# Performance work log

Hardware: AMD Instinct MI355X
Metric: run time of the kernel (lower is better)

Reference implementation:

```python
import jax, jax.numpy as jnp
import numpy as np

B, N, IN_FEAT, OUT_FEAT, FEAT_DIM, N_HEAD = 16, 1024, 64, 128, 64, 4
NEG_SLOPE = 0.2


def setup_inputs() -> dict:
    key = jax.random.key(0)
    k1, k2, k3, k4 = jax.random.split(key, 4)
    # xavier-uniform-ish init, gain folded into scale
    def xav(k, shape):
        fan_in, fan_out = shape[-2], shape[-1]
        lim = 1.414 * np.sqrt(6.0 / (fan_in + fan_out))
        return jax.random.uniform(k, shape, jnp.float32, -lim, lim)
    return {
        "h": jax.random.normal(k1, (B, N, IN_FEAT), jnp.float32),
        "mask": jnp.ones((B, 1, N, N), jnp.float32),
        "w": xav(k2, (N_HEAD, IN_FEAT, OUT_FEAT)),
        "a_src": xav(k3, (N_HEAD, OUT_FEAT, FEAT_DIM)),
        "a_dst": xav(k4, (N_HEAD, OUT_FEAT, FEAT_DIM)),
        "bias": jnp.zeros((OUT_FEAT,), jnp.float32),
    }


def reference(h, mask, w, a_src, a_dst, bias):
    # h: [B,N,F_in]; w: [H,F_in,F_out] -> h_prime: [B,H,N,F_out]
    h_prime = jnp.einsum('bnf,hfo->bhno', h, w)
    attn_src = jnp.einsum('bhno,hod->bhnd', h_prime, a_src)  # [B,H,N,D]
    attn_dst = jnp.einsum('bhno,hod->bhnd', h_prime, a_dst)  # [B,H,N,D]
    scores = jnp.einsum('bhnd,bhmd->bhnm', attn_src, attn_dst)  # [B,H,N,N]
    attn = jax.nn.softmax(jax.nn.leaky_relu(scores, NEG_SLOPE), axis=-1)
    # dropout is identity in eval mode (deterministic reference)
    attn = attn * mask  # mask broadcast over heads
    out = jnp.einsum('bhnm,bhmo->bno', attn, h_prime) + bias  # sum over heads
    out = out + h_prime.sum(axis=1)  # skip connection
    return out, attn
```

## Files before the change

kernel.cpp:

```cpp
#include <hip/hip_runtime.h>

#define BB 16
#define NN 1024
#define FIN 64
#define FOUT 128
#define DD 64
#define HH 4
#define NEG 0.2f

#define RT 32
#define RT2 16
#define CT 128

typedef __attribute__((ext_vector_type(8))) short short8;
typedef __attribute__((ext_vector_type(4))) float f32x4;

__device__ __forceinline__ unsigned short f2bf(float x) {
    union { float f; unsigned u; } v; v.f = x;
    unsigned r = v.u + 0x7fffu + ((v.u >> 16) & 1u);
    return (unsigned short)(r >> 16);
}
__device__ __forceinline__ float bf2f(unsigned short s) {
    union { float f; unsigned u; } v; v.u = ((unsigned)s) << 16;
    return v.f;
}

#define MFMA(a, b, c) __builtin_amdgcn_mfma_f32_16x16x32_bf16((a), (b), (c), 0, 0, 0)

__global__ __launch_bounds__(256) void gat_k1(
    const float* __restrict__ h,
    const float* __restrict__ w,
    const float* __restrict__ a_src,
    const float* __restrict__ a_dst,
    unsigned short* __restrict__ asHg,
    unsigned short* __restrict__ asLg,
    unsigned short* __restrict__ adHg,
    unsigned short* __restrict__ adLg,
    unsigned short* __restrict__ hpPg,
    float* __restrict__ hpsum)
{
    __shared__ float hL[RT][FIN + 1];
    __shared__ float wL[FIN][FOUT + 2];
    __shared__ float hpL[RT][FOUT + 2];

    const int t  = threadIdx.x;
    const int tx = t & 31;
    const int ty = t >> 5;
    const int blk = blockIdx.x;
    const int b   = blk / (NN / RT);
    const int n0  = (blk % (NN / RT)) * RT;

    for (int idx = t; idx < RT * FIN / 4; idx += 256) {
        int r = (idx * 4) / FIN;
        int f = (idx * 4) % FIN;
        float4 v = *reinterpret_cast<const float4*>(&h[((size_t)b * NN + n0 + r) * FIN + f]);
        hL[r][f + 0] = v.x; hL[r][f + 1] = v.y; hL[r][f + 2] = v.z; hL[r][f + 3] = v.w;
    }

    float sum_acc[4][4];
#pragma unroll
    for (int i = 0; i < 4; i++)
#pragma unroll
        for (int j = 0; j < 4; j++) sum_acc[i][j] = 0.f;

    for (int hh = 0; hh < HH; ++hh) {
        __syncthreads();
        for (int idx = t; idx < FIN * FOUT / 4; idx += 256) {
            int k = (idx * 4) / FOUT;
            int o = (idx * 4) % FOUT;
            float4 v = *reinterpret_cast<const float4*>(&w[((size_t)hh * FIN + k) * FOUT + o]);
            wL[k][o + 0] = v.x; wL[k][o + 1] = v.y; wL[k][o + 2] = v.z; wL[k][o + 3] = v.w;
        }
        __syncthreads();

        float acc[4][4];
#pragma unroll
        for (int i = 0; i < 4; i++)
#pragma unroll
            for (int j = 0; j < 4; j++) acc[i][j] = 0.f;

#pragma unroll 8
        for (int k = 0; k < FIN; k++) {
            float av0 = hL[ty][k], av1 = hL[ty + 8][k], av2 = hL[ty + 16][k], av3 = hL[ty + 24][k];
            float bv0 = wL[k][tx], bv1 = wL[k][tx + 32], bv2 = wL[k][tx + 64], bv3 = wL[k][tx + 96];
            acc[0][0] += av0 * bv0; acc[0][1] += av0 * bv1; acc[0][2] += av0 * bv2; acc[0][3] += av0 * bv3;
            acc[1][0] += av1 * bv0; acc[1][1] += av1 * bv1; acc[1][2] += av1 * bv2; acc[1][3] += av1 * bv3;
            acc[2][0] += av2 * bv0; acc[2][1] += av2 * bv1; acc[2][2] += av2 * bv2; acc[2][3] += av2 * bv3;
            acc[3][0] += av3 * bv0; acc[3][1] += av3 * bv1; acc[3][2] += av3 * bv2; acc[3][3] += av3 * bv3;
        }

        const size_t bh = (size_t)b * HH + hh;
#pragma unroll
        for (int i = 0; i < 4; i++) {
            int r = i * 8 + ty;
#pragma unroll
            for (int j = 0; j < 4; j++) {
                int o = j * 32 + tx;
                hpL[r][o] = acc[i][j];
                sum_acc[i][j] += acc[i][j];
            }
        }
        __syncthreads();

        float as0[4], as1[4], ad0[4], ad1[4];
#pragma unroll
        for (int i = 0; i < 4; i++) { as0[i] = 0.f; as1[i] = 0.f; ad0[i] = 0.f; ad1[i] = 0.f; }

#pragma unroll 4
        for (int o = 0; o < FOUT; o++) {
            size_t aoff = ((size_t)hh * FOUT + o) * DD;
            float sv0 = a_src[aoff + tx];
            float sv1 = a_src[aoff + tx + 32];
            float dv0 = a_dst[aoff + tx];
            float dv1 = a_dst[aoff + tx + 32];
#pragma unroll
            for (int i = 0; i < 4; i++) {
                float hv = hpL[i * 8 + ty][o];
                as0[i] += hv * sv0; as1[i] += hv * sv1;
                ad0[i] += hv * dv0; ad1[i] += hv * dv1;
            }
        }
#pragma unroll
        for (int i = 0; i < 4; i++) {
            int r = i * 8 + ty;
            size_t base = (bh * NN + n0 + r) * DD;
            unsigned short h0, h1;
            h0 = f2bf(as0[i]); asHg[base + tx]      = h0; asLg[base + tx]      = f2bf(as0[i] - bf2f(h0));
            h1 = f2bf(as1[i]); asHg[base + tx + 32] = h1; asLg[base + tx + 32] = f2bf(as1[i] - bf2f(h1));
            h0 = f2bf(ad0[i]); adHg[base + tx]      = h0; adLg[base + tx]      = f2bf(ad0[i] - bf2f(h0));
            h1 = f2bf(ad1[i]); adHg[base + tx + 32] = h1; adLg[base + tx + 32] = f2bf(ad1[i] - bf2f(h1));
        }

        {
            int o = t & 127, half = t >> 7;
            size_t dst = ((bh * (NN / 32) + (n0 >> 5)) * FOUT + o) * 32 + half * 16;
            short8 v0, v1;
#pragma unroll
            for (int k = 0; k < 8; k++) v0[k] = (short)f2bf(hpL[half * 16 + k][o]);
#pragma unroll
            for (int k = 0; k < 8; k++) v1[k] = (short)f2bf(hpL[half * 16 + 8 + k][o]);
            *reinterpret_cast<short8*>(&hpPg[dst])     = v0;
            *reinterpret_cast<short8*>(&hpPg[dst + 8]) = v1;
        }
    }

#pragma unroll
    for (int i = 0; i < 4; i++) {
        int r = i * 8 + ty;
        size_t rowoff = ((size_t)b * NN + n0 + r) * FOUT;
#pragma unroll
        for (int j = 0; j < 4; j++) {
            hpsum[rowoff + j * 32 + tx] = sum_acc[i][j];
        }
    }
}

__global__ __launch_bounds__(256) void gat_k2(
    const float* __restrict__ mask,
    const float* __restrict__ bias,
    const unsigned short* __restrict__ asHg,
    const unsigned short* __restrict__ asLg,
    const unsigned short* __restrict__ adHg,
    const unsigned short* __restrict__ adLg,
    const unsigned short* __restrict__ hpPg,
    const float* __restrict__ hpsum,
    float* __restrict__ out,
    float* __restrict__ attn)
{
    __shared__ __align__(16) unsigned char smem[8192 + 512];
    unsigned short* pBs0 = reinterpret_cast<unsigned short*>(smem);
    unsigned short* pBs1 = reinterpret_cast<unsigned short*>(smem + 4096);
    float*          redm = reinterpret_cast<float*>(smem + 8192);
    float*          redl = reinterpret_cast<float*>(smem + 8192 + 256);
    float*          outL = reinterpret_cast<float*>(smem);

    const int t  = threadIdx.x;
    const int l  = t & 63;
    const int w  = t >> 6;
    const int li = l & 15;
    const int g  = l >> 4;

    const int lb = (blockIdx.x & 7) * 128 + (blockIdx.x >> 3);
    const int b  = lb >> 6;
    const int n0 = (lb & 63) * RT2;

    f32x4 oacc[2];
    oacc[0] = f32x4{0.f, 0.f, 0.f, 0.f};
    oacc[1] = f32x4{0.f, 0.f, 0.f, 0.f};

    for (int hh = 0; hh < HH; hh++) {
        const size_t bh = (size_t)b * HH + hh;

        short8 aH[2], aL[2];
#pragma unroll
        for (int ks = 0; ks < 2; ks++) {
            size_t src = (bh * NN + n0 + li) * DD + ks * 32 + g * 8;
            aH[ks] = *reinterpret_cast<const short8*>(&asHg[src]);
            aL[ks] = *reinterpret_cast<const short8*>(&asLg[src]);
        }

        const unsigned short* adHb = adHg + bh * NN * DD;
        const unsigned short* adLb = adLg + bh * NN * DD;

        float sc[8][2][4];
#pragma unroll
        for (int ct = 0; ct < 8; ct++) {
#pragma unroll
            for (int cf = 0; cf < 2; cf++) {
                short8 bHr[2], bLr[2];
#pragma unroll
                for (int ks = 0; ks < 2; ks++) {
                    size_t off = (size_t)(ct * CT + w * 32 + cf * 16 + li) * DD + ks * 32 + g * 8;
                    bHr[ks] = *reinterpret_cast<const short8*>(&adHb[off]);
                    bLr[ks] = *reinterpret_cast<const short8*>(&adLb[off]);
                }
                f32x4 s = f32x4{0.f, 0.f, 0.f, 0.f};
                __builtin_amdgcn_s_setprio(1);
#pragma unroll
                for (int ks = 0; ks < 2; ks++) {
                    s = MFMA(aH[ks], bHr[ks], s);
                    s = MFMA(aH[ks], bLr[ks], s);
                    s = MFMA(aL[ks], bHr[ks], s);
                }
                __builtin_amdgcn_s_setprio(0);
#pragma unroll
                for (int q = 0; q < 4; q++) {
                    float v = s[q];
                    sc[ct][cf][q] = v > 0.f ? v : NEG * v;
                }
            }
        }

        float mreg[4];
#pragma unroll
        for (int q = 0; q < 4; q++) {
            float m = sc[0][0][q];
#pragma unroll
            for (int ct = 0; ct < 8; ct++)
                m = fmaxf(m, fmaxf(sc[ct][0][q], sc[ct][1][q]));
#pragma unroll
            for (int msk = 1; msk < 16; msk <<= 1)
                m = fmaxf(m, __shfl_xor(m, msk));
            mreg[q] = m;
        }
        __syncthreads();
        if (li == 0) {
#pragma unroll
            for (int q = 0; q < 4; q++) redm[w * 16 + g * 4 + q] = mreg[q];
        }
        __syncthreads();
        float mf[4];
#pragma unroll
        for (int q = 0; q < 4; q++) {
            int row = g * 4 + q;
            mf[q] = fmaxf(fmaxf(redm[row], redm[16 + row]),
                          fmaxf(redm[32 + row], redm[48 + row]));
        }
        float lreg[4] = {0.f, 0.f, 0.f, 0.f};
#pragma unroll
        for (int ct = 0; ct < 8; ct++)
#pragma unroll
            for (int cf = 0; cf < 2; cf++)
#pragma unroll
                for (int q = 0; q < 4; q++) {
                    float e = __expf(sc[ct][cf][q] - mf[q]);
                    sc[ct][cf][q] = e;
                    lreg[q] += e;
                }
#pragma unroll
        for (int q = 0; q < 4; q++) {
#pragma unroll
            for (int msk = 1; msk < 16; msk <<= 1)
                lreg[q] += __shfl_xor(lreg[q], msk);
        }
        if (li == 0) {
#pragma unroll
            for (int q = 0; q < 4; q++) redl[w * 16 + g * 4 + q] = lreg[q];
        }
        __syncthreads();
        float linv[4];
#pragma unroll
        for (int q = 0; q < 4; q++) {
            int row = g * 4 + q;
            linv[q] = 1.0f / (redl[row] + redl[16 + row] + redl[32 + row] + redl[48 + row]);
        }

        const unsigned short* hpbase = hpPg + bh * (size_t)(NN / 32) * FOUT * 32;
#pragma unroll
        for (int ct = 0; ct < 8; ct++) {
            float mvv[2][4];
#pragma unroll
            for (int cf = 0; cf < 2; cf++)
#pragma unroll
                for (int q = 0; q < 4; q++)
                    mvv[cf][q] = mask[((size_t)b * NN + n0 + g * 4 + q) * NN
                                      + ct * CT + w * 32 + cf * 16 + li];

            unsigned short* pB = (ct & 1) ? pBs1 : pBs0;
            float pm[2][4];
#pragma unroll
            for (int cf = 0; cf < 2; cf++)
#pragma unroll
                for (int q = 0; q < 4; q++) {
                    int row = g * 4 + q;
                    int cl  = w * 32 + cf * 16 + li;
                    float pmv = sc[ct][cf][q] * linv[q] * mvv[cf][q];
                    attn[(bh * NN + n0 + row) * NN + ct * CT + cl] = pmv;
                    pm[cf][q] = pmv;
                }
#pragma unroll
            for (int cf = 0; cf < 2; cf++)
#pragma unroll
                for (int q = 0; q < 4; q++) {
                    int row = g * 4 + q;
                    int cl  = w * 32 + cf * 16 + li;
                    pB[row * 128 + (cl ^ (row * 8))] = f2bf(pm[cf][q]);
                }

            const unsigned short* hpb = hpbase + (size_t)ct * 4 * FOUT * 32;
            short8 hbv[4][2];
#pragma unroll
            for (int kc = 0; kc < 4; kc++) {
                hbv[kc][0] = *reinterpret_cast<const short8*>(
                    &hpb[((size_t)kc * FOUT + w * 32 + li) * 32 + g * 8]);
                hbv[kc][1] = *reinterpret_cast<const short8*>(
                    &hpb[((size_t)kc * FOUT + w * 32 + 16 + li) * 32 + g * 8]);
            }
            asm volatile("s_waitcnt lgkmcnt(0)\n\ts_barrier" ::: "memory");

#pragma unroll
            for (int kc = 0; kc < 4; kc++) {
                int k = kc * 32 + g * 8;
                short8 pa = *reinterpret_cast<const short8*>(&pB[li * 128 + (k ^ (li * 8))]);
                __builtin_amdgcn_s_setprio(1);
                oacc[0] = MFMA(pa, hbv[kc][0], oacc[0]);
                oacc[1] = MFMA(pa, hbv[kc][1], oacc[1]);
                __builtin_amdgcn_s_setprio(0);
            }
        }
    }

    __syncthreads();
#pragma unroll
    for (int of = 0; of < 2; of++)
#pragma unroll
        for (int q = 0; q < 4; q++) {
            int row = g * 4 + q;
            int col = w * 32 + of * 16 + li;
            outL[row * 128 + col] = oacc[of][q];
        }
    __syncthreads();
    {
        int row = t >> 4, cb = (t & 15) * 8;
        size_t obase = ((size_t)b * NN + n0 + row) * FOUT + cb;
#pragma unroll
        for (int k4 = 0; k4 < 2; k4++) {
            float4 v  = *reinterpret_cast<float4*>(&outL[row * 128 + cb + k4 * 4]);
            float4 bs = *reinterpret_cast<const float4*>(&bias[cb + k4 * 4]);
            float4 hs = *reinterpret_cast<const float4*>(&hpsum[obase + k4 * 4]);
            v.x += bs.x + hs.x; v.y += bs.y + hs.y; v.z += bs.z + hs.z; v.w += bs.w + hs.w;
            *reinterpret_cast<float4*>(&out[obase + k4 * 4]) = v;
        }
    }
}

extern "C" void kernel_launch(void* const* d_in, const int* in_sizes, int n_in,
                              void* d_out, int out_size, void* d_ws, size_t ws_size,
                              hipStream_t stream) {
    const float* h      = (const float*)d_in[0];
    const float* mask   = (const float*)d_in[1];
    const float* w      = (const float*)d_in[2];
    const float* a_src  = (const float*)d_in[3];
    const float* a_dst  = (const float*)d_in[4];
    const float* bias   = (const float*)d_in[5];

    float* out  = (float*)d_out;
    float* attn = out + (size_t)BB * NN * FOUT;

    const size_t NASD = (size_t)BB * HH * NN * DD;
    unsigned short* asHg = (unsigned short*)d_ws;
    unsigned short* asLg = asHg + NASD;
    unsigned short* adHg = asLg + NASD;
    unsigned short* adLg = adHg + NASD;
    unsigned short* hpPg = adLg + NASD;
    float* hpsum = (float*)(hpPg + (size_t)BB * HH * FOUT * NN);

    dim3 block(256);
    gat_k1<<<dim3(BB * (NN / RT)),  block, 0, stream>>>(h, w, a_src, a_dst, asHg, asLg, adHg, adLg, hpPg, hpsum);
    gat_k2<<<dim3(BB * (NN / RT2)), block, 0, stream>>>(mask, bias, asHg, asLg, adHg, adLg, hpPg, hpsum, out, attn);
}
```

Measured before the change: 387.3 us.

## Use online softmax with bf16-packed exponentials and transposed score MFMA in attention kernel

Swaps the score MFMA operands so each lane owns one query row, which allows float4 mask loads and float4 attn stores. Replaces the two-pass max/sum reduction with an online per-tile max and rescaled sum, merged across lanes and waves as (max, sum) pairs in a single shared-memory round. Keeps the exponentials packed as bf16 to cut register use and adds a launch bound of 3 blocks per SM. It also splits the h' loads so half are issued inside the MFMA loop. The aim is higher occupancy, fewer barriers and wider global stores, at the cost of bf16 rounding of the exponentials before they are written to attn.

```diff
diff --git a/kernel.cpp b/kernel.cpp
--- a/kernel.cpp
+++ b/kernel.cpp
@@ -23,6 +23,9 @@
 __device__ __forceinline__ float bf2f(unsigned short s) {
     union { float f; unsigned u; } v; v.u = ((unsigned)s) << 16;
     return v.f;
+}
+__device__ __forceinline__ unsigned pack2bf(float lo, float hi) {
+    return (unsigned)f2bf(lo) | ((unsigned)f2bf(hi) << 16);
 }
 
 #define MFMA(a, b, c) __builtin_amdgcn_mfma_f32_16x16x32_bf16((a), (b), (c), 0, 0, 0)
@@ -155,7 +158,7 @@
     }
 }
 
-__global__ __launch_bounds__(256) void gat_k2(
+__global__ __launch_bounds__(256, 3) void gat_k2(
     const float* __restrict__ mask,
     const float* __restrict__ bias,
     const unsigned short* __restrict__ asHg,
@@ -170,8 +173,7 @@
     __shared__ __align__(16) unsigned char smem[8192 + 512];
     unsigned short* pBs0 = reinterpret_cast<unsigned short*>(smem);
     unsigned short* pBs1 = reinterpret_cast<unsigned short*>(smem + 4096);
-    float*          redm = reinterpret_cast<float*>(smem + 8192);
-    float*          redl = reinterpret_cast<float*>(smem + 8192 + 256);
+    float2*         red  = reinterpret_cast<float2*>(smem + 8192);
     float*          outL = reinterpret_cast<float*>(smem);
 
     const int t  = threadIdx.x;
@@ -179,6 +181,7 @@
     const int w  = t >> 6;
     const int li = l & 15;
     const int g  = l >> 4;
+    const int colb = w * 32;
 
     const int lb = (blockIdx.x & 7) * 128 + (blockIdx.x >> 3);
     const int b  = lb >> 6;
@@ -202,134 +205,114 @@
         const unsigned short* adHb = adHg + bh * NN * DD;
         const unsigned short* adLb = adLg + bh * NN * DD;
 
-        float sc[8][2][4];
+        float m = -3.0e38f, lsum = 0.f;
+        float mL[8];
+        unsigned pk[8][2][2];
 #pragma unroll
         for (int ct = 0; ct < 8; ct++) {
+            float sv[2][4];
 #pragma unroll
             for (int cf = 0; cf < 2; cf++) {
-                short8 bHr[2], bLr[2];
+                short8 xH[2], xL[2];
 #pragma unroll
                 for (int ks = 0; ks < 2; ks++) {
-                    size_t off = (size_t)(ct * CT + w * 32 + cf * 16 + li) * DD + ks * 32 + g * 8;
-                    bHr[ks] = *reinterpret_cast<const short8*>(&adHb[off]);
-                    bLr[ks] = *reinterpret_cast<const short8*>(&adLb[off]);
+                    size_t off = (size_t)(ct * CT + colb + cf * 16 + li) * DD + ks * 32 + g * 8;
+                    xH[ks] = *reinterpret_cast<const short8*>(&adHb[off]);
+                    xL[ks] = *reinterpret_cast<const short8*>(&adLb[off]);
                 }
                 f32x4 s = f32x4{0.f, 0.f, 0.f, 0.f};
                 __builtin_amdgcn_s_setprio(1);
 #pragma unroll
                 for (int ks = 0; ks < 2; ks++) {
-                    s = MFMA(aH[ks], bHr[ks], s);
-                    s = MFMA(aH[ks], bLr[ks], s);
-                    s = MFMA(aL[ks], bHr[ks], s);
+                    s = MFMA(xH[ks], aH[ks], s);
+                    s = MFMA(xH[ks], aL[ks], s);
+                    s = MFMA(xL[ks], aH[ks], s);
                 }
                 __builtin_amdgcn_s_setprio(0);
 #pragma unroll
                 for (int q = 0; q < 4; q++) {
                     float v = s[q];
-                    sc[ct][cf][q] = v > 0.f ? v : NEG * v;
+                    sv[cf][q] = v > 0.f ? v : NEG * v;
                 }
             }
-        }
-
-        float mreg[4];
-#pragma unroll
-        for (int q = 0; q < 4; q++) {
-            float m = sc[0][0][q];
-#pragma unroll
-            for (int ct = 0; ct < 8; ct++)
-                m = fmaxf(m, fmaxf(sc[ct][0][q], sc[ct][1][q]));
-#pragma unroll
-            for (int msk = 1; msk < 16; msk <<= 1)
-                m = fmaxf(m, __shfl_xor(m, msk));
-            mreg[q] = m;
-        }
-        __syncthreads();
-        if (li == 0) {
-#pragma unroll
-            for (int q = 0; q < 4; q++) redm[w * 16 + g * 4 + q] = mreg[q];
-        }
-        __syncthreads();
-        float mf[4];
-#pragma unroll
-        for (int q = 0; q < 4; q++) {
-            int row = g * 4 + q;
-            mf[q] = fmaxf(fmaxf(redm[row], redm[16 + row]),
-                          fmaxf(redm[32 + row], redm[48 + row]));
-        }
-        float lreg[4] = {0.f, 0.f, 0.f, 0.f};
-#pragma unroll
-        for (int ct = 0; ct < 8; ct++)
+            float tm = sv[0][0];
 #pragma unroll
             for (int cf = 0; cf < 2; cf++)
 #pragma unroll
-                for (int q = 0; q < 4; q++) {
-                    float e = __expf(sc[ct][cf][q] - mf[q]);
-                    sc[ct][cf][q] = e;
-                    lreg[q] += e;
-                }
-#pragma unroll
-        for (int q = 0; q < 4; q++) {
-#pragma unroll
-            for (int msk = 1; msk < 16; msk <<= 1)
-                lreg[q] += __shfl_xor(lreg[q], msk);
-        }
-        if (li == 0) {
-#pragma unroll
-            for (int q = 0; q < 4; q++) redl[w * 16 + g * 4 + q] = lreg[q];
-        }
-        __syncthreads();
-        float linv[4];
-#pragma unroll
-        for (int q = 0; q < 4; q++) {
-            int row = g * 4 + q;
-            linv[q] = 1.0f / (redl[row] + redl[16 + row] + redl[32 + row] + redl[48 + row]);
+                for (int q = 0; q < 4; q++) tm = fmaxf(tm, sv[cf][q]);
+            float nm = fmaxf(m, tm);
+            lsum *= __expf(m - nm);
+            m = nm;
+            mL[ct] = nm;
+#pragma unroll
+            for (int cf = 0; cf < 2; cf++) {
+                float e0 = __expf(sv[cf][0] - nm);
+                float e1 = __expf(sv[cf][1] - nm);
+                float e2 = __expf(sv[cf][2] - nm);
+                float e3 = __expf(sv[cf][3] - nm);
+                lsum += (e0 + e1) + (e2 + e3);
+                pk[ct][cf][0] = pack2bf(e0, e1);
+                pk[ct][cf][1] = pack2bf(e2, e3);
+            }
+        }
+
+#pragma unroll
+        for (int msk = 16; msk <= 32; msk <<= 1) {
+            float om = __shfl_xor(m, msk);
+            float ol = __shfl_xor(lsum, msk);
+            float nm = fmaxf(m, om);
+            lsum = lsum * __expf(m - nm) + ol * __expf(om - nm);
+            m = nm;
+        }
+        __syncthreads();
+        if (g == 0) red[w * 16 + li] = make_float2(m, lsum);
+        __syncthreads();
+        float mf, linv;
+        {
+            float2 r0 = red[li], r1 = red[16 + li], r2 = red[32 + li], r3 = red[48 + li];
+            mf = fmaxf(fmaxf(r0.x, r1.x), fmaxf(r2.x, r3.x));
+            float ls = r0.y * __expf(r0.x - mf) + r1.y * __expf(r1.x - mf)
+                     + r2.y * __expf(r2.x - mf) + r3.y * __expf(r3.x - mf);
+            linv = 1.0f / ls;
         }
 
         const unsigned short* hpbase = hpPg + bh * (size_t)(NN / 32) * FOUT * 32;
 #pragma unroll
         for (int ct = 0; ct < 8; ct++) {
-            float mvv[2][4];
-#pragma unroll
-            for (int cf = 0; cf < 2; cf++)
-#pragma unroll
-                for (int q = 0; q < 4; q++)
-                    mvv[cf][q] = mask[((size_t)b * NN + n0 + g * 4 + q) * NN
-                                      + ct * CT + w * 32 + cf * 16 + li];
-
+            const float corr = __expf(mL[ct] - mf) * linv;
             unsigned short* pB = (ct & 1) ? pBs1 : pBs0;
-            float pm[2][4];
-#pragma unroll
-            for (int cf = 0; cf < 2; cf++)
-#pragma unroll
-                for (int q = 0; q < 4; q++) {
-                    int row = g * 4 + q;
-                    int cl  = w * 32 + cf * 16 + li;
-                    float pmv = sc[ct][cf][q] * linv[q] * mvv[cf][q];
-                    attn[(bh * NN + n0 + row) * NN + ct * CT + cl] = pmv;
-                    pm[cf][q] = pmv;
-                }
-#pragma unroll
-            for (int cf = 0; cf < 2; cf++)
-#pragma unroll
-                for (int q = 0; q < 4; q++) {
-                    int row = g * 4 + q;
-                    int cl  = w * 32 + cf * 16 + li;
-                    pB[row * 128 + (cl ^ (row * 8))] = f2bf(pm[cf][q]);
-                }
+#pragma unroll
+            for (int cf = 0; cf < 2; cf++) {
+                int c = ct * CT + colb + cf * 16 + g * 4;
+                float4 mv = *reinterpret_cast<const float4*>(
+                    &mask[((size_t)b * NN + n0 + li) * NN + c]);
+                float p0 = bf2f((unsigned short)(pk[ct][cf][0] & 0xffff)) * corr * mv.x;
+                float p1 = bf2f((unsigned short)(pk[ct][cf][0] >> 16))    * corr * mv.y;
+                float p2 = bf2f((unsigned short)(pk[ct][cf][1] & 0xffff)) * corr * mv.z;
+                float p3 = bf2f((unsigned short)(pk[ct][cf][1] >> 16))    * corr * mv.w;
+                float4 av; av.x = p0; av.y = p1; av.z = p2; av.w = p3;
+                *reinterpret_cast<float4*>(
+                    &attn[(bh * NN + n0 + li) * NN + c]) = av;
+                int c0 = colb + cf * 16 + g * 4;
+                uint2 pw;
+                pw.x = pack2bf(p0, p1);
+                pw.y = pack2bf(p2, p3);
+                *reinterpret_cast<uint2*>(&pB[li * 128 + (c0 ^ (li * 8))]) = pw;
+            }
 
             const unsigned short* hpb = hpbase + (size_t)ct * 4 * FOUT * 32;
-            short8 hbv[4][2];
-#pragma unroll
-            for (int kc = 0; kc < 4; kc++) {
+            short8 hbv[2][2];
+#pragma unroll
+            for (int kc = 0; kc < 2; kc++) {
                 hbv[kc][0] = *reinterpret_cast<const short8*>(
-                    &hpb[((size_t)kc * FOUT + w * 32 + li) * 32 + g * 8]);
+                    &hpb[((size_t)kc * FOUT + colb + li) * 32 + g * 8]);
                 hbv[kc][1] = *reinterpret_cast<const short8*>(
-                    &hpb[((size_t)kc * FOUT + w * 32 + 16 + li) * 32 + g * 8]);
+                    &hpb[((size_t)kc * FOUT + colb + 16 + li) * 32 + g * 8]);
             }
             asm volatile("s_waitcnt lgkmcnt(0)\n\ts_barrier" ::: "memory");
 
 #pragma unroll
-            for (int kc = 0; kc < 4; kc++) {
+            for (int kc = 0; kc < 2; kc++) {
                 int k = kc * 32 + g * 8;
                 short8 pa = *reinterpret_cast<const short8*>(&pB[li * 128 + (k ^ (li * 8))]);
                 __builtin_amdgcn_s_setprio(1);
@@ -337,6 +320,19 @@
                 oacc[1] = MFMA(pa, hbv[kc][1], oacc[1]);
                 __builtin_amdgcn_s_setprio(0);
             }
+#pragma unroll
+            for (int kc = 2; kc < 4; kc++) {
+                int k = kc * 32 + g * 8;
+                short8 pa = *reinterpret_cast<const short8*>(&pB[li * 128 + (k ^ (li * 8))]);
+                short8 h0 = *reinterpret_cast<const short8*>(
+                    &hpb[((size_t)kc * FOUT + colb + li) * 32 + g * 8]);
+                short8 h1 = *reinterpret_cast<const short8*>(
+                    &hpb[((size_t)kc * FOUT + colb + 16 + li) * 32 + g * 8]);
+                __builtin_amdgcn_s_setprio(1);
+                oacc[0] = MFMA(pa, h0, oacc[0]);
+                oacc[1] = MFMA(pa, h1, oacc[1]);
+                __builtin_amdgcn_s_setprio(0);
+            }
         }
     }
 
@@ -346,7 +342,7 @@
 #pragma unroll
         for (int q = 0; q < 4; q++) {
             int row = g * 4 + q;
-            int col = w * 32 + of * 16 + li;
+            int col = colb + of * 16 + li;
             outL[row * 128 + col] = oacc[of][q];
         }
     __syncthreads();
```

Result: slower. 604.3 us (+56.0%).
